# Performance work log

Hardware: AMD Instinct MI355X
Metric: run time of the kernel (lower is better)

Reference implementation:

```python
import jax, jax.numpy as jnp
import numpy as np


def _chamfer(samp_pc, ref_pc):
    """Squared-L2 chamfer: returns (cost_p1_p2 [B,N], cost_p2_p1 [B,M]).

    samp_pc: [B, N, 3], ref_pc: [B, M, 3]
    """
    s2 = jnp.sum(samp_pc * samp_pc, axis=-1)  # [B, N]
    r2 = jnp.sum(ref_pc * ref_pc, axis=-1)    # [B, M]
    cross = jnp.einsum('bnd,bmd->bnm', samp_pc, ref_pc)  # [B, N, M]
    d2 = s2[:, :, None] + r2[:, None, :] - 2.0 * cross   # [B, N, M]
    d2 = jnp.maximum(d2, 0.0)  # numerical floor
    cost_p1_p2 = jnp.min(d2, axis=2)  # [B, N] nearest ref for each samp point
    cost_p2_p1 = jnp.min(d2, axis=1)  # [B, M] nearest samp for each ref point
    return cost_p1_p2, cost_p2_p1


def setup_inputs() -> dict:
    key = jax.random.key(0)
    k1, k2 = jax.random.split(key)
    B, N, M = 16, 2048, 8192
    ref_pc = jax.random.normal(k1, (B, M, 3), dtype=jnp.float32)
    samp_pc = jax.random.normal(k2, (B, N, 3), dtype=jnp.float32)
    return {"ref_pc": ref_pc, "samp_pc": samp_pc}


def reference(ref_pc, samp_pc):
    cost_p1_p2, cost_p2_p1 = _chamfer(samp_pc, ref_pc)
    cd_p = (jnp.sqrt(cost_p1_p2).mean(axis=1) + jnp.sqrt(cost_p2_p1).mean(axis=1)) / 2.0
    cd_t = cost_p1_p2.mean(axis=1) + cost_p2_p1.mean(axis=1)
    return (cd_p, cd_t)
```

## Files before the change

### kernel.cpp

```cpp
#include <hip/hip_runtime.h>
#include <math.h>

#define BB 16
#define NN 2048
#define MM 8192

#define BLK 256
#define R 4
#define G (BLK * R)
#define YS (MM / G)
#define QCH 64
#define ZS (NN / QCH)
#define QPH 16
#define PHASES (QCH / QPH)

typedef float v2f __attribute__((ext_vector_type(2)));

static __device__ __forceinline__ v2f v2_splat(float s) { v2f r; r.x = s; r.y = s; return r; }
static __device__ __forceinline__ v2f v2_fma(v2f a, v2f b, v2f c) {
#if __has_builtin(__builtin_elementwise_fma)
    return __builtin_elementwise_fma(a, b, c);
#else
    v2f r; r.x = fmaf(a.x, b.x, c.x); r.y = fmaf(a.y, b.y, c.y); return r;
#endif
}


__global__ void __launch_bounds__(BLK) prep_kernel(const float* __restrict__ ref,
                                                   const float* __restrict__ samp,
                                                   float4* __restrict__ ref4,
                                                   float4* __restrict__ samp_pk,
                                                   unsigned int* __restrict__ ws2,
                                                   float* __restrict__ out) {
    int i = blockIdx.x * blockDim.x + threadIdx.x;
    const int PM = BB * MM;
    const int PPAIR = BB * NN / 2;
    if (i < 2 * BB) out[i] = 0.f;
    if (i < PM) {
        float p1 = ref[(size_t)i * 3 + 0], p2 = ref[(size_t)i * 3 + 1], p3 = ref[(size_t)i * 3 + 2];
        float q = fmaf(p1, p1, fmaf(p2, p2, p3 * p3));
        ref4[i] = make_float4(-2.f * p1, -2.f * p2, -2.f * p3, q);
        ws2[i] = 0x7F800000u;
    } else if (i < PM + PPAIR) {
        int k = i - PM;
        const float* s0 = samp + (size_t)k * 6;
        float x0 = s0[0], y0 = s0[1], z0 = s0[2];
        float x1 = s0[3], y1 = s0[4], z1 = s0[5];
        float w0 = fmaf(x0, x0, fmaf(y0, y0, z0 * z0));
        float w1 = fmaf(x1, x1, fmaf(y1, y1, z1 * z1));
        samp_pk[(size_t)k * 2 + 0] = make_float4(x0, x1, y0, y1);
        samp_pk[(size_t)k * 2 + 1] = make_float4(z0, z1, w0, w1);
    }
}

__global__ void __launch_bounds__(BLK) sweep_kernel(const float4* __restrict__ ref4,
                                                    const float4* __restrict__ samp_pk,
                                                    unsigned int* __restrict__ ws2,
                                                    float* __restrict__ ws1p) {
    __shared__ v2f tqbuf[(QPH / 2) * BLK];
    const int b = blockIdx.x;
    const int lane = threadIdx.x & 63;
    const int wv = threadIdx.x >> 6;
    const int refbase = blockIdx.y * G + wv * (64 * R);

    const float4* rp = ref4 + (size_t)b * MM + refbase;
    float px[R], py[R], pz[R], pp[R], mref[R];
#pragma unroll
    for (int r = 0; r < R; ++r) {
        float4 v = rp[r * 64 + lane];
        px[r] = v.x; py[r] = v.y; pz[r] = v.z; pp[r] = v.w;
        mref[r] = INFINITY;
    }

    const int q0 = blockIdx.z * QCH;
    const float4* qt = samp_pk + (size_t)b * NN + q0;
    float* w1 = ws1p + (size_t)blockIdx.y * (BB * NN) + (size_t)b * NN + q0;

    for (int ph = 0; ph < PHASES; ++ph) {
        const float4* qp = qt + ph * QPH;

#pragma unroll 4
        for (int j = 0; j < QPH / 2; ++j) {
            float4 a = qp[2 * j];
            float4 c = qp[2 * j + 1];
            v2f qx; qx.x = a.x; qx.y = a.y;
            v2f qy; qy.x = a.z; qy.y = a.w;
            v2f qz; qz.x = c.x; qz.y = c.y;
            v2f qw; qw.x = c.z; qw.y = c.w;
            v2f t[R];
#pragma unroll
            for (int r = 0; r < R; ++r) {
                v2f s = v2_fma(v2_splat(px[r]), qx, v2_splat(pp[r]));
                s = v2_fma(v2_splat(py[r]), qy, s);
                s = v2_fma(v2_splat(pz[r]), qz, s);
                t[r] = s + qw;
            }
#pragma unroll
            for (int r = 0; r < R; ++r)
                mref[r] = fminf(fminf(mref[r], t[r].x), t[r].y);
            v2f o;
            o.x = fminf(fminf(fminf(t[0].x, t[1].x), t[2].x), t[3].x);
            o.y = fminf(fminf(fminf(t[0].y, t[1].y), t[2].y), t[3].y);
            tqbuf[j * BLK + threadIdx.x] = o;
        }
        __syncthreads();

#pragma unroll
        for (int jj = 0; jj < (QPH / 2) / 4; ++jj) {
            const int jp = wv * ((QPH / 2) / 4) + jj;
            const v2f* s2 = tqbuf + jp * BLK;
            v2f v0 = s2[lane], v1 = s2[lane + 64], v2_ = s2[lane + 128], v3 = s2[lane + 192];
            float m0 = fminf(fminf(fminf(v0.x, v1.x), v2_.x), v3.x);
            float m1 = fminf(fminf(fminf(v0.y, v1.y), v2_.y), v3.y);
#pragma unroll
            for (int s = 32; s > 0; s >>= 1) {
                m0 = fminf(m0, __shfl_xor(m0, s));
                m1 = fminf(m1, __shfl_xor(m1, s));
            }
            if (lane == 0) {
                float2 st; st.x = m0; st.y = m1;
                *(float2*)(w1 + ph * QPH + 2 * jp) = st;
            }
        }
        __syncthreads();
    }

    unsigned int* w2 = ws2 + (size_t)b * MM + refbase;
#pragma unroll
    for (int r = 0; r < R; ++r)
        atomicMin(&w2[r * 64 + lane], __float_as_uint(fmaxf(mref[r], 0.f)));
}

#define BLKR 256
__global__ void __launch_bounds__(BLKR) reduce_kernel(const float* __restrict__ ws1p,
                                                      const unsigned int* __restrict__ ws2,
                                                      float* __restrict__ out) {
    const int b = blockIdx.x;
    const int qtr = blockIdx.y;
    const int tid = threadIdx.x;

    float sd1 = 0.f, sr1 = 0.f;
    for (int i = qtr * (NN / 4) + tid; i < (qtr + 1) * (NN / 4); i += BLKR) {
        float m = INFINITY;
#pragma unroll
        for (int y = 0; y < YS; ++y)
            m = fminf(m, ws1p[(size_t)y * (BB * NN) + (size_t)b * NN + i]);
        float v = fmaxf(m, 0.f);
        sd1 += v;
        sr1 += sqrtf(v);
    }
    float sd2 = 0.f, sr2 = 0.f;
    for (int i = qtr * (MM / 4) + tid; i < (qtr + 1) * (MM / 4); i += BLKR) {
        float v = __uint_as_float(ws2[(size_t)b * MM + i]);
        sd2 += v;
        sr2 += sqrtf(v);
    }

    __shared__ float4 red[BLKR];
    red[tid] = make_float4(sd1, sr1, sd2, sr2);
    __syncthreads();
    for (int s = BLKR / 2; s > 0; s >>= 1) {
        if (tid < s) {
            red[tid].x += red[tid + s].x;
            red[tid].y += red[tid + s].y;
            red[tid].z += red[tid + s].z;
            red[tid].w += red[tid + s].w;
        }
        __syncthreads();
    }
    if (tid == 0) {
        float4 r = red[0];
        atomicAdd(&out[b],      (r.y * (1.0f / NN) + r.w * (1.0f / MM)) * 0.5f);
        atomicAdd(&out[BB + b],  r.x * (1.0f / NN) + r.z * (1.0f / MM));
    }
}

extern "C" void kernel_launch(void* const* d_in, const int* in_sizes, int n_in,
                              void* d_out, int out_size, void* d_ws, size_t ws_size,
                              hipStream_t stream) {
    const float* ref  = (const float*)d_in[0];
    const float* samp = (const float*)d_in[1];
    float* out = (float*)d_out;

    float4* ref4    = (float4*)d_ws;
    float4* samp_pk = ref4 + (size_t)BB * MM;
    unsigned int* ws2 = (unsigned int*)(samp_pk + (size_t)BB * NN);
    float* ws1p = (float*)(ws2 + (size_t)BB * MM);

    const int P = BB * MM + BB * NN / 2;
    prep_kernel<<<(P + BLK - 1) / BLK, BLK, 0, stream>>>(ref, samp, ref4, samp_pk, ws2, out);

    dim3 gs(BB, YS, ZS);
    sweep_kernel<<<gs, BLK, 0, stream>>>(ref4, samp_pk, ws2, ws1p);

    dim3 gr(BB, 4);
    reduce_kernel<<<gr, BLKR, 0, stream>>>(ws1p, ws2, out);
}
```

Measured before the change: 103.9 us.

## Replace LDS cross-wave min reduction with DPP wave reduce and global atomicMin

```diff
diff --git a/kernel.cpp b/kernel.cpp
--- a/kernel.cpp
+++ b/kernel.cpp
@@ -9,10 +9,9 @@
 #define R 4
 #define G (BLK * R)
 #define YS (MM / G)
-#define QCH 64
+#define QCH 32
 #define ZS (NN / QCH)
-#define QPH 16
-#define PHASES (QCH / QPH)
+#define NPAIR (QCH / 2)
 
 typedef float v2f __attribute__((ext_vector_type(2)));
 
@@ -25,17 +24,39 @@
 #endif
 }
 
+#define DPP_ROW_SHR(n) (0x110 | (n))
+#define DPP_ROW_BCAST15 0x142
+#define DPP_ROW_BCAST31 0x143
+
+template <int CTRL>
+static __device__ __forceinline__ float dpp_min_step(float v) {
+    int b = __float_as_int(v);
+    int s = __builtin_amdgcn_update_dpp(b, b, CTRL, 0xf, 0xf, false);
+    return fminf(v, __int_as_float(s));
+}
+static __device__ __forceinline__ float wave_min_dpp(float v) {
+    v = dpp_min_step<DPP_ROW_SHR(1)>(v);
+    v = dpp_min_step<DPP_ROW_SHR(2)>(v);
+    v = dpp_min_step<DPP_ROW_SHR(4)>(v);
+    v = dpp_min_step<DPP_ROW_SHR(8)>(v);
+    v = dpp_min_step<DPP_ROW_BCAST15>(v);
+    v = dpp_min_step<DPP_ROW_BCAST31>(v);
+    return v;
+}
+
 
 __global__ void __launch_bounds__(BLK) prep_kernel(const float* __restrict__ ref,
                                                    const float* __restrict__ samp,
                                                    float4* __restrict__ ref4,
                                                    float4* __restrict__ samp_pk,
                                                    unsigned int* __restrict__ ws2,
+                                                   unsigned int* __restrict__ ws1,
                                                    float* __restrict__ out) {
     int i = blockIdx.x * blockDim.x + threadIdx.x;
     const int PM = BB * MM;
     const int PPAIR = BB * NN / 2;
     if (i < 2 * BB) out[i] = 0.f;
+    if (i < BB * NN) ws1[i] = 0x7F800000u;
     if (i < PM) {
         float p1 = ref[(size_t)i * 3 + 0], p2 = ref[(size_t)i * 3 + 1], p3 = ref[(size_t)i * 3 + 2];
         float q = fmaf(p1, p1, fmaf(p2, p2, p3 * p3));
@@ -56,8 +77,7 @@
 __global__ void __launch_bounds__(BLK) sweep_kernel(const float4* __restrict__ ref4,
                                                     const float4* __restrict__ samp_pk,
                                                     unsigned int* __restrict__ ws2,
-                                                    float* __restrict__ ws1p) {
-    __shared__ v2f tqbuf[(QPH / 2) * BLK];
+                                                    unsigned int* __restrict__ ws1) {
     const int b = blockIdx.x;
     const int lane = threadIdx.x & 63;
     const int wv = threadIdx.x >> 6;
@@ -74,55 +94,35 @@
 
     const int q0 = blockIdx.z * QCH;
     const float4* qt = samp_pk + (size_t)b * NN + q0;
-    float* w1 = ws1p + (size_t)blockIdx.y * (BB * NN) + (size_t)b * NN + q0;
-
-    for (int ph = 0; ph < PHASES; ++ph) {
-        const float4* qp = qt + ph * QPH;
+    unsigned int* w1 = ws1 + (size_t)b * NN + q0;
 
 #pragma unroll 4
-        for (int j = 0; j < QPH / 2; ++j) {
-            float4 a = qp[2 * j];
-            float4 c = qp[2 * j + 1];
-            v2f qx; qx.x = a.x; qx.y = a.y;
-            v2f qy; qy.x = a.z; qy.y = a.w;
-            v2f qz; qz.x = c.x; qz.y = c.y;
-            v2f qw; qw.x = c.z; qw.y = c.w;
-            v2f t[R];
+    for (int j = 0; j < NPAIR; ++j) {
+        float4 a = qt[2 * j];
+        float4 c = qt[2 * j + 1];
+        v2f qx; qx.x = a.x; qx.y = a.y;
+        v2f qy; qy.x = a.z; qy.y = a.w;
+        v2f qz; qz.x = c.x; qz.y = c.y;
+        v2f qw; qw.x = c.z; qw.y = c.w;
+        v2f t[R];
 #pragma unroll
-            for (int r = 0; r < R; ++r) {
-                v2f s = v2_fma(v2_splat(px[r]), qx, v2_splat(pp[r]));
-                s = v2_fma(v2_splat(py[r]), qy, s);
-                s = v2_fma(v2_splat(pz[r]), qz, s);
-                t[r] = s + qw;
-            }
+        for (int r = 0; r < R; ++r) {
+            v2f s = v2_fma(v2_splat(px[r]), qx, v2_splat(pp[r]));
+            s = v2_fma(v2_splat(py[r]), qy, s);
+            s = v2_fma(v2_splat(pz[r]), qz, s);
+            t[r] = s + qw;
+        }
 #pragma unroll
-            for (int r = 0; r < R; ++r)
-                mref[r] = fminf(fminf(mref[r], t[r].x), t[r].y);
-            v2f o;
-            o.x = fminf(fminf(fminf(t[0].x, t[1].x), t[2].x), t[3].x);
-            o.y = fminf(fminf(fminf(t[0].y, t[1].y), t[2].y), t[3].y);
-            tqbuf[j * BLK + threadIdx.x] = o;
+        for (int r = 0; r < R; ++r)
+            mref[r] = fminf(fminf(mref[r], t[r].x), t[r].y);
+        float ox = fminf(fminf(fminf(t[0].x, t[1].x), t[2].x), t[3].x);
+        float oy = fminf(fminf(fminf(t[0].y, t[1].y), t[2].y), t[3].y);
+        ox = wave_min_dpp(ox);
+        oy = wave_min_dpp(oy);
+        if (lane == 63) {
+            atomicMin(&w1[2 * j],     __float_as_uint(fmaxf(ox, 0.f)));
+            atomicMin(&w1[2 * j + 1], __float_as_uint(fmaxf(oy, 0.f)));
         }
-        __syncthreads();
-
-#pragma unroll
-        for (int jj = 0; jj < (QPH / 2) / 4; ++jj) {
-            const int jp = wv * ((QPH / 2) / 4) + jj;
-            const v2f* s2 = tqbuf + jp * BLK;
-            v2f v0 = s2[lane], v1 = s2[lane + 64], v2_ = s2[lane + 128], v3 = s2[lane + 192];
-            float m0 = fminf(fminf(fminf(v0.x, v1.x), v2_.x), v3.x);
-            float m1 = fminf(fminf(fminf(v0.y, v1.y), v2_.y), v3.y);
-#pragma unroll
-            for (int s = 32; s > 0; s >>= 1) {
-                m0 = fminf(m0, __shfl_xor(m0, s));
-                m1 = fminf(m1, __shfl_xor(m1, s));
-            }
-            if (lane == 0) {
-                float2 st; st.x = m0; st.y = m1;
-                *(float2*)(w1 + ph * QPH + 2 * jp) = st;
-            }
-        }
-        __syncthreads();
     }
 
     unsigned int* w2 = ws2 + (size_t)b * MM + refbase;
@@ -132,7 +132,7 @@
 }
 
 #define BLKR 256
-__global__ void __launch_bounds__(BLKR) reduce_kernel(const float* __restrict__ ws1p,
+__global__ void __launch_bounds__(BLKR) reduce_kernel(const unsigned int* __restrict__ ws1,
                                                       const unsigned int* __restrict__ ws2,
                                                       float* __restrict__ out) {
     const int b = blockIdx.x;
@@ -141,11 +141,7 @@
 
     float sd1 = 0.f, sr1 = 0.f;
     for (int i = qtr * (NN / 4) + tid; i < (qtr + 1) * (NN / 4); i += BLKR) {
-        float m = INFINITY;
-#pragma unroll
-        for (int y = 0; y < YS; ++y)
-            m = fminf(m, ws1p[(size_t)y * (BB * NN) + (size_t)b * NN + i]);
-        float v = fmaxf(m, 0.f);
+        float v = __uint_as_float(ws1[(size_t)b * NN + i]);
         sd1 += v;
         sr1 += sqrtf(v);
     }
@@ -185,14 +181,14 @@
     float4* ref4    = (float4*)d_ws;
     float4* samp_pk = ref4 + (size_t)BB * MM;
     unsigned int* ws2 = (unsigned int*)(samp_pk + (size_t)BB * NN);
-    float* ws1p = (float*)(ws2 + (size_t)BB * MM);
+    unsigned int* ws1 = ws2 + (size_t)BB * MM;
 
     const int P = BB * MM + BB * NN / 2;
-    prep_kernel<<<(P + BLK - 1) / BLK, BLK, 0, stream>>>(ref, samp, ref4, samp_pk, ws2, out);
+    prep_kernel<<<(P + BLK - 1) / BLK, BLK, 0, stream>>>(ref, samp, ref4, samp_pk, ws2, ws1, out);
 
     dim3 gs(BB, YS, ZS);
-    sweep_kernel<<<gs, BLK, 0, stream>>>(ref4, samp_pk, ws2, ws1p);
+    sweep_kernel<<<gs, BLK, 0, stream>>>(ref4, samp_pk, ws2, ws1);
 
     dim3 gr(BB, 4);
-    reduce_kernel<<<gr, BLKR, 0, stream>>>(ws1p, ws2, out);
+    reduce_kernel<<<gr, BLKR, 0, stream>>>(ws1, ws2, out);
 }
```

After: 259.8 us. 2.5x slower.
